# Performance work log

Measured on AMD Instinct MI355X. Metric: run time of the kernel, lower is better.

Reference implementation:

```python
import jax, jax.numpy as jnp
import numpy as np

EPS = 1e-5

def _bn(y, gamma, beta):
    # BatchNorm1d in training mode over the flattened (B*N, C) batch dim.
    m = jnp.mean(y, axis=0)
    v = jnp.var(y, axis=0)  # biased variance, matches torch normalization
    return gamma * (y - m) * jax.lax.rsqrt(v + EPS) + beta

def _hardswish(x):
    return x * jnp.clip(x + 3.0, 0.0, 6.0) / 6.0

def setup_inputs() -> dict:
    key = jax.random.key(0)
    ks = jax.random.split(key, 8)
    B, N, C, H = 16, 784, 384, 8
    res = int(N ** 0.5)  # 28
    inner = 3 * C
    x = jax.random.normal(ks[0], (B, N, C), dtype=jnp.float32)
    Wqkv = jax.random.normal(ks[1], (inner, C), dtype=jnp.float32) * (C ** -0.5)
    g1 = jnp.ones((inner,), jnp.float32) + 0.1 * jax.random.normal(ks[2], (inner,))
    b1 = 0.1 * jax.random.normal(ks[3], (inner,))
    Wproj = jax.random.normal(ks[4], (C, C), dtype=jnp.float32) * (C ** -0.5)
    g2 = jnp.ones((C,), jnp.float32) + 0.1 * jax.random.normal(ks[5], (C,))
    b2 = 0.1 * jax.random.normal(ks[6], (C,))
    biases = 0.02 * jax.random.normal(ks[7], (H, res * res), dtype=jnp.float32)
    # idx[i,j] = |dx|*res + |dy| reproduces torch's encounter-order offset ids
    coords = np.stack(np.meshgrid(np.arange(res), np.arange(res), indexing='ij'), -1).reshape(N, 2)
    d = np.abs(coords[:, None, :] - coords[None, :, :])
    bias_idxs = jnp.asarray(d[..., 0] * res + d[..., 1], dtype=jnp.int32)  # [N,N]
    return {"x": x, "Wqkv": Wqkv, "g1": g1, "b1": b1, "Wproj": Wproj,
            "g2": g2, "b2": b2, "biases": biases, "bias_idxs": bias_idxs}

def reference(x, Wqkv, g1, b1, Wproj, g2, b2, biases, bias_idxs):
    B, N, C = x.shape
    H = biases.shape[0]
    hd = C // H
    scale = hd ** -0.5
    # qkv = LinearNorm(dim, 3*dim)
    y = _bn(x.reshape(B * N, C) @ Wqkv.T, g1, b1)              # [B*N, 3C]
    qkv = y.reshape(B, N, 3, H, hd).transpose(2, 0, 3, 1, 4)   # [3,B,H,N,hd]
    q, k, v = qkv[0], qkv[1], qkv[2]
    attn = jnp.einsum('bhnd,bhmd->bhnm', q, k) * scale         # [B,H,N,N]
    attn = attn + biases[:, bias_idxs][None]                   # gathered rel-pos bias
    attn = jax.nn.softmax(attn, axis=-1)
    o = jnp.einsum('bhnm,bhmd->bhnd', attn, v)                 # [B,H,N,hd]
    o = o.transpose(0, 2, 1, 3).reshape(B, N, C)
    # proj = Hardswish -> LinearNorm(dim, dim)
    o = _hardswish(o).reshape(B * N, C)
    o = _bn(o @ Wproj.T, g2, b2)
    return o.reshape(B, N, C)
```

## Files before the change

### kernel.cpp

```cpp
#include <hip/hip_runtime.h>

#define R_TOTAL 12544
#define NTOK    784
#define CDIM    384
#define INNER   1152
#define NHEAD   8
#define HDIM    48
#define BATCH   16
#define SCALE   0.14433756729740643f
#define INV28   0.035714287f

typedef unsigned short u16;
typedef unsigned int   u32;
typedef __attribute__((ext_vector_type(8))) short short8;
typedef __attribute__((ext_vector_type(4))) float floatx4;

union V8 { uint4 u; short8 s; u16 h[8]; };

#define OB_OFF     28901376ull
#define ST_OFF     38535168ull

__device__ __forceinline__ float b2f(u16 u) {
    union { float f; u32 i; } v; v.i = ((u32)u) << 16; return v.f;
}
__device__ __forceinline__ u16 f2b(float f) {
    union { float f; u32 i; } v; v.f = f;
    u32 r = v.i + 0x7FFFu + ((v.i >> 16) & 1u);
    return (u16)(r >> 16);
}
__device__ __forceinline__ u32 pk2(float lo, float hi) {
    return (u32)f2b(lo) | ((u32)f2b(hi) << 16);
}
__device__ __forceinline__ float hswish_f(float v) {
    return v * fminf(fmaxf(v + 3.f, 0.f), 6.f) * (1.f / 6.f);
}

__global__ __launch_bounds__(256) void zero_k(float* __restrict__ p, int n) {
    int i = blockIdx.x * 256 + threadIdx.x;
    if (i < n) p[i] = 0.f;
}

template<int ABF16, int HSW, int OBF16>
__global__ __launch_bounds__(256) void gemm_mfma_k(
    const void* __restrict__ Ap, const float* __restrict__ Bfp,
    void* __restrict__ Cp, float* __restrict__ sums, int M, int Nout, int K)
{
    __shared__ u16 As[128 * 40];
    __shared__ u16 Bs[128 * 40];
    const int t = threadIdx.x;
    const int lane = t & 63, wv = t >> 6;
    const int l15 = lane & 15, quad = lane >> 4;
    const int wm = (wv & 1) * 64, wn = (wv >> 1) * 64;
    const int m0 = blockIdx.y * 128, n0 = blockIdx.x * 128;
    const floatx4 zf = {0.f, 0.f, 0.f, 0.f};

    floatx4 acc[4][4];
    #pragma unroll
    for (int i = 0; i < 4; i++)
        #pragma unroll
        for (int j = 0; j < 4; j++) acc[i][j] = zf;

    for (int k0 = 0; k0 < K; k0 += 32) {
        __syncthreads();
        #pragma unroll
        for (int it = 0; it < 2; it++) {
            const int flat = t + it * 256;
            const int rr = flat >> 2, ss = (flat & 3) * 8;
            uint4 aw;
            if (ABF16) {
                uint4 u = *(const uint4*)((const u16*)Ap + (size_t)(m0 + rr) * K + k0 + ss);
                if (HSW) {
                    aw.x = pk2(hswish_f(b2f((u16)(u.x & 0xffff))), hswish_f(b2f((u16)(u.x >> 16))));
                    aw.y = pk2(hswish_f(b2f((u16)(u.y & 0xffff))), hswish_f(b2f((u16)(u.y >> 16))));
                    aw.z = pk2(hswish_f(b2f((u16)(u.z & 0xffff))), hswish_f(b2f((u16)(u.z >> 16))));
                    aw.w = pk2(hswish_f(b2f((u16)(u.w & 0xffff))), hswish_f(b2f((u16)(u.w >> 16))));
                } else {
                    aw = u;
                }
            } else {
                const float* p = (const float*)Ap + (size_t)(m0 + rr) * K + k0 + ss;
                float4 f0 = *(const float4*)p, f1 = *(const float4*)(p + 4);
                aw.x = pk2(f0.x, f0.y); aw.y = pk2(f0.z, f0.w);
                aw.z = pk2(f1.x, f1.y); aw.w = pk2(f1.z, f1.w);
            }
            *(uint4*)&As[rr * 40 + ss] = aw;
            const float* q = Bfp + (size_t)(n0 + rr) * K + k0 + ss;
            float4 g0 = *(const float4*)q, g1 = *(const float4*)(q + 4);
            uint4 bw;
            bw.x = pk2(g0.x, g0.y); bw.y = pk2(g0.z, g0.w);
            bw.z = pk2(g1.x, g1.y); bw.w = pk2(g1.z, g1.w);
            *(uint4*)&Bs[rr * 40 + ss] = bw;
        }
        __syncthreads();
        short8 af[4], bfr[4];
        #pragma unroll
        for (int mi = 0; mi < 4; mi++)
            af[mi] = *(const short8*)&As[(wm + mi * 16 + l15) * 40 + quad * 8];
        #pragma unroll
        for (int ni = 0; ni < 4; ni++)
            bfr[ni] = *(const short8*)&Bs[(wn + ni * 16 + l15) * 40 + quad * 8];
        #pragma unroll
        for (int mi = 0; mi < 4; mi++)
            #pragma unroll
            for (int ni = 0; ni < 4; ni++)
                acc[mi][ni] = __builtin_amdgcn_mfma_f32_16x16x32_bf16(af[mi], bfr[ni], acc[mi][ni], 0, 0, 0);
    }

    float cs[4] = {0.f, 0.f, 0.f, 0.f}, cq[4] = {0.f, 0.f, 0.f, 0.f};
    #pragma unroll
    for (int mi = 0; mi < 4; mi++) {
        const int mbase = m0 + wm + mi * 16 + quad * 4;
        #pragma unroll
        for (int ni = 0; ni < 4; ni++) {
            const int n = n0 + wn + ni * 16 + l15;
            #pragma unroll
            for (int reg = 0; reg < 4; reg++) {
                size_t off = (size_t)(mbase + reg) * Nout + n;
                float v = acc[mi][ni][reg];
                float vv;
                if (OBF16) {
                    u16 hv = f2b(v);
                    ((u16*)Cp)[off] = hv;
                    vv = b2f(hv);
                } else {
                    ((float*)Cp)[off] = v;
                    vv = v;
                }
                cs[ni] += vv;
                cq[ni] += vv * vv;
            }
        }
    }
    #pragma unroll
    for (int ni = 0; ni < 4; ni++) {
        float s = cs[ni], sq = cq[ni];
        s  += __shfl_xor(s, 16);  s  += __shfl_xor(s, 32);
        sq += __shfl_xor(sq, 16); sq += __shfl_xor(sq, 32);
        if (quad == 0) {
            int col = n0 + wn + ni * 16 + l15;
            atomicAdd(&sums[col], s);
            atomicAdd(&sums[Nout + col], sq);
        }
    }
}

__global__ __launch_bounds__(256) void finalize_bn_k(
    const float* __restrict__ sums, const float* __restrict__ g,
    const float* __restrict__ bvec, float* __restrict__ ab, int Ncols, float invM)
{
    int c = blockIdx.x * 256 + threadIdx.x;
    if (c >= Ncols) return;
    float mean = sums[c] * invM;
    float var  = sums[Ncols + c] * invM - mean * mean;
    float a    = g[c] * rsqrtf(var + 1e-5f);
    ab[c] = a;
    ab[Ncols + c] = bvec[c] - mean * a;
}

__global__ __launch_bounds__(256) void bn_apply_k(
    float* __restrict__ Z, const float* __restrict__ ab, int Ncols, int total4)
{
    for (int i4 = blockIdx.x * 256 + threadIdx.x; i4 < total4; i4 += gridDim.x * 256) {
        int col = (i4 * 4) % Ncols;
        float4 z  = *(float4*)(Z + (size_t)i4 * 4);
        float4 a4 = *(const float4*)(ab + col);
        float4 b4 = *(const float4*)(ab + Ncols + col);
        z.x = a4.x * z.x + b4.x; z.y = a4.y * z.y + b4.y;
        z.z = a4.z * z.z + b4.z; z.w = a4.w * z.w + b4.w;
        *(float4*)(Z + (size_t)i4 * 4) = z;
    }
}

__global__ __launch_bounds__(256) void bn_apply_bf16_k(
    u16* __restrict__ Z, const float* __restrict__ ab, int Ncols, int total8)
{
    int i8 = blockIdx.x * 256 + threadIdx.x;
    if (i8 >= total8) return;
    int col = (i8 * 8) % Ncols;
    uint4 u = *(uint4*)(Z + (size_t)i8 * 8);
    float4 A0 = *(const float4*)(ab + col),         A1 = *(const float4*)(ab + col + 4);
    float4 B0 = *(const float4*)(ab + Ncols + col), B1 = *(const float4*)(ab + Ncols + col + 4);
    uint4 o;
    o.x = pk2(fmaf(b2f((u16)(u.x & 0xffff)), A0.x, B0.x), fmaf(b2f((u16)(u.x >> 16)), A0.y, B0.y));
    o.y = pk2(fmaf(b2f((u16)(u.y & 0xffff)), A0.z, B0.z), fmaf(b2f((u16)(u.y >> 16)), A0.w, B0.w));
    o.z = pk2(fmaf(b2f((u16)(u.z & 0xffff)), A1.x, B1.x), fmaf(b2f((u16)(u.z >> 16)), A1.y, B1.y));
    o.w = pk2(fmaf(b2f((u16)(u.w & 0xffff)), A1.z, B1.z), fmaf(b2f((u16)(u.w >> 16)), A1.w, B1.w));
    *(uint4*)(Z + (size_t)i8 * 8) = o;
}

__device__ __forceinline__ uint4 transpose8x8_u16(uint4 v, int g) {
    u32 r0 = v.x, r1 = v.y, r2 = v.z, r3 = v.w;
    {
        u32 t0 = (u32)__shfl_xor((int)r2, 4);
        u32 t1 = (u32)__shfl_xor((int)r3, 4);
        u32 t2 = (u32)__shfl_xor((int)r0, 4);
        u32 t3 = (u32)__shfl_xor((int)r1, 4);
        bool gb2 = (g >> 2) & 1;
        r0 = gb2 ? t0 : r0;
        r1 = gb2 ? t1 : r1;
        r2 = gb2 ? r2 : t2;
        r3 = gb2 ? r3 : t3;
    }
    {
        u32 t0 = (u32)__shfl_xor((int)r1, 2);
        u32 t1 = (u32)__shfl_xor((int)r0, 2);
        u32 t2 = (u32)__shfl_xor((int)r3, 2);
        u32 t3 = (u32)__shfl_xor((int)r2, 2);
        bool gb1 = (g >> 1) & 1;
        r0 = gb1 ? t0 : r0;
        r1 = gb1 ? r1 : t1;
        r2 = gb1 ? t2 : r2;
        r3 = gb1 ? r3 : t3;
    }
    {
        u32 t0 = (u32)__shfl_xor((int)r0, 1);
        u32 t1 = (u32)__shfl_xor((int)r1, 1);
        u32 t2 = (u32)__shfl_xor((int)r2, 1);
        u32 t3 = (u32)__shfl_xor((int)r3, 1);
        if (g & 1) {
            r0 = (r0 & 0xFFFF0000u) | (t0 >> 16);
            r1 = (r1 & 0xFFFF0000u) | (t1 >> 16);
            r2 = (r2 & 0xFFFF0000u) | (t2 >> 16);
            r3 = (r3 & 0xFFFF0000u) | (t3 >> 16);
        } else {
            r0 = (r0 & 0x0000FFFFu) | (t0 << 16);
            r1 = (r1 & 0x0000FFFFu) | (t1 << 16);
            r2 = (r2 & 0x0000FFFFu) | (t2 << 16);
            r3 = (r3 & 0x0000FFFFu) | (t3 << 16);
        }
    }
    return make_uint4(r0, r1, r2, r3);
}

__global__ __launch_bounds__(256) void attn_mfma_k(
    const u16* __restrict__ Y,
    const float* __restrict__ biases,
    u16* __restrict__ O)
{
    __shared__ u16 vt[2][6 * 64 * 8];
    __shared__ u16 psm[4][2][2 * 64 * 8];
    __shared__ float hb[NTOK];

    const int t = threadIdx.x;
    const int lane = t & 63, wv = t >> 6;
    const int l15 = lane & 15, quad = lane >> 4;
    const int g8 = lane & 7, sg = lane >> 3;
    const int bh = blockIdx.x;
    const int b = bh >> 3, h = bh & 7;
    const int n0 = blockIdx.y * 128;
    const int bN = b * NTOK;
    const int colQ = h * HDIM, colK = CDIM + colQ, colV = 2 * CDIM + colQ;
    const floatx4 zf = {0.f, 0.f, 0.f, 0.f};

    if (t < 196) *(float4*)&hb[t << 2] = *(const float4*)(biases + (size_t)h * NTOK + (t << 2));

    int qv[2], qr[2], xi[2], yi[2];
    #pragma unroll
    for (int qh = 0; qh < 2; qh++) {
        qv[qh] = n0 + qh * 64 + wv * 16 + l15;
        qr[qh] = qv[qh] < NTOK ? qv[qh] : NTOK - 1;
        xi[qh] = (int)((float)qr[qh] * INV28);
        yi[qh] = qr[qh] - 28 * xi[qh];
    }

    short8 qf[2][2];
    #pragma unroll
    for (int qh = 0; qh < 2; qh++) {
        V8 a0, a1;
        a1.u = make_uint4(0u, 0u, 0u, 0u);
        const u16* src = Y + (size_t)(bN + qr[qh]) * INNER + colQ;
        a0.u = *(const uint4*)(src + quad * 8);
        if (quad < 2) a1.u = *(const uint4*)(src + 32 + quad * 8);
        qf[qh][0] = a0.s; qf[qh][1] = a1.s;
    }

    const bool ownB = (wv < 2);
    const int dsA = wv, dsB = 4 + wv;
    const int dA = dsA * 8 + g8, dB = dsB * 8 + g8;
    const int vaddrA = (((dA >> 4) * 2 + (sg >> 2)) * 64 + (sg & 3) * 16 + (dA & 15)) * 8;
    const int vaddrB = (((dB >> 4) * 2 + (sg >> 2)) * 64 + (sg & 3) * 16 + (dB & 15)) * 8;

    V8 pvA, pvB;
    {
        const u16* src = Y + (size_t)(bN + lane) * INNER + colV;
        pvA.u = *(const uint4*)(src + dsA * 8);
        if (ownB) pvB.u = *(const uint4*)(src + dsB * 8);
        *(uint4*)&vt[0][vaddrA] = transpose8x8_u16(pvA.u, g8);
        if (ownB) *(uint4*)&vt[0][vaddrB] = transpose8x8_u16(pvB.u, g8);
    }

    V8 kfr[4][2];
    #pragma unroll
    for (int sub = 0; sub < 4; sub++) {
        const u16* src = Y + (size_t)(bN + sub * 16 + l15) * INNER + colK;
        kfr[sub][0].u = *(const uint4*)(src + quad * 8);
        kfr[sub][1].u = *(const uint4*)(src + 32 + quad * 8);
    }

    float lsum[2] = {0.f, 0.f};
    floatx4 oacc[2][3];
    #pragma unroll
    for (int qh = 0; qh < 2; qh++)
        #pragma unroll
        for (int i = 0; i < 3; i++) oacc[qh][i] = zf;

    const int psbase = ((quad >> 1) * 16 + l15) * 8 + (quad & 1) * 4;

    for (int mt = 0; mt < 13; mt++) {
        const int m0k = mt * 64;
        __syncthreads();

        V8 kn[4][2];
        const bool more = (mt + 1 < 13);
        if (more) {
            const int mn = m0k + 64;
            #pragma unroll
            for (int sub = 0; sub < 4; sub++) {
                int key = mn + sub * 16 + l15;
                int kr  = key < NTOK ? key : NTOK - 1;
                const u16* src = Y + (size_t)(bN + kr) * INNER + colK;
                kn[sub][0].u = *(const uint4*)(src + quad * 8);
                kn[sub][1].u = *(const uint4*)(src + 32 + quad * 8);
            }
            int kv = mn + lane; kv = kv < NTOK ? kv : NTOK - 1;
            const u16* src = Y + (size_t)(bN + kv) * INNER + colV;
            pvA.u = *(const uint4*)(src + dsA * 8);
            if (ownB) pvB.u = *(const uint4*)(src + dsB * 8);
        }

        #pragma unroll
        for (int qh = 0; qh < 2; qh++) {
            floatx4 sf[4];
            #pragma unroll
            for (int sub = 0; sub < 4; sub++) {
                floatx4 c = zf;
                c = __builtin_amdgcn_mfma_f32_16x16x32_bf16(kfr[sub][0].s, qf[qh][0], c, 0, 0, 0);
                c = __builtin_amdgcn_mfma_f32_16x16x32_bf16(kfr[sub][1].s, qf[qh][1], c, 0, 0, 0);
                sf[sub] = c;
            }
            #pragma unroll
            for (int sub = 0; sub < 4; sub++) {
                int kb = m0k + sub * 16 + quad * 4;
                float pr[4];
                #pragma unroll
                for (int reg = 0; reg < 4; reg++) {
                    int key = kb + reg;
                    int xk = (int)((float)key * INV28);
                    int yk = key - 28 * xk;
                    int dx = xi[qh] - xk; dx = dx < 0 ? -dx : dx;
                    int dy = yi[qh] - yk; dy = dy < 0 ? -dy : dy;
                    float p = 0.f;
                    if (key < NTOK)
                        p = __expf(fmaf(sf[sub][reg], SCALE, hb[dx * 28 + dy]));
                    pr[reg] = p;
                    lsum[qh] += p;
                }
                int addr = psbase + (sub >> 1) * 512 + (sub & 1) * 256;
                *(uint2*)&psm[wv][qh][addr] = make_uint2(pk2(pr[0], pr[1]), pk2(pr[2], pr[3]));
            }
        }

        if (more) {
            u16* vtb = vt[(mt + 1) & 1];
            *(uint4*)&vtb[vaddrA] = transpose8x8_u16(pvA.u, g8);
            if (ownB) *(uint4*)&vtb[vaddrB] = transpose8x8_u16(pvB.u, g8);
        }

        const u16* vtb = vt[mt & 1];
        #pragma unroll
        for (int kc = 0; kc < 2; kc++) {
            short8 pb0 = *(const short8*)&psm[wv][0][(kc * 64 + lane) * 8];
            short8 pb1 = *(const short8*)&psm[wv][1][(kc * 64 + lane) * 8];
            #pragma unroll
            for (int ns = 0; ns < 3; ns++) {
                short8 va = *(const short8*)&vtb[((ns * 2 + kc) * 64 + lane) * 8];
                oacc[0][ns] = __builtin_amdgcn_mfma_f32_16x16x32_bf16(va, pb0, oacc[0][ns], 0, 0, 0);
                oacc[1][ns] = __builtin_amdgcn_mfma_f32_16x16x32_bf16(va, pb1, oacc[1][ns], 0, 0, 0);
            }
        }

        if (more) {
            #pragma unroll
            for (int sub = 0; sub < 4; sub++) {
                kfr[sub][0] = kn[sub][0];
                kfr[sub][1] = kn[sub][1];
            }
        }
    }

    #pragma unroll
    for (int qh = 0; qh < 2; qh++) {
        float ls = lsum[qh];
        ls += __shfl_xor(ls, 16);
        ls += __shfl_xor(ls, 32);
        if (qv[qh] < NTOK) {
            float rl = 1.f / ls;
            u16* dst = O + (size_t)(bN + qv[qh]) * CDIM + colQ;
            #pragma unroll
            for (int ns = 0; ns < 3; ns++)
                #pragma unroll
                for (int reg = 0; reg < 4; reg++)
                    dst[ns * 16 + quad * 4 + reg] = f2b(hswish_f(oacc[qh][ns][reg] * rl));
        }
    }
}

extern "C" void kernel_launch(void* const* d_in, const int* in_sizes, int n_in,
                              void* d_out, int out_size, void* d_ws, size_t ws_size,
                              hipStream_t stream)
{
    const float* x     = (const float*)d_in[0];
    const float* Wqkv  = (const float*)d_in[1];
    const float* g1    = (const float*)d_in[2];
    const float* b1    = (const float*)d_in[3];
    const float* Wproj = (const float*)d_in[4];
    const float* g2    = (const float*)d_in[5];
    const float* b2    = (const float*)d_in[6];
    const float* bias  = (const float*)d_in[7];
    float* out = (float*)d_out;
    char*  wsb = (char*)d_ws;

    u16*   Yb  = (u16*)wsb;
    u16*   Ob  = (u16*)(wsb + OB_OFF);
    float* S1  = (float*)(wsb + ST_OFF);
    float* AB1 = S1 + 2304;
    float* S2  = AB1 + 2304;
    float* AB2 = S2 + 768;

    zero_k<<<24, 256, 0, stream>>>(S1, 6144);

    gemm_mfma_k<0, 0, 1><<<dim3(INNER / 128, R_TOTAL / 128), 256, 0, stream>>>(
        x, Wqkv, Yb, S1, R_TOTAL, INNER, CDIM);

    finalize_bn_k<<<(INNER + 255) / 256, 256, 0, stream>>>(S1, g1, b1, AB1, INNER, 1.f / R_TOTAL);
    bn_apply_bf16_k<<<(R_TOTAL * INNER / 8 + 255) / 256, 256, 0, stream>>>(
        Yb, AB1, INNER, R_TOTAL * INNER / 8);

    attn_mfma_k<<<dim3(NHEAD * BATCH, 7), 256, 0, stream>>>(Yb, bias, Ob);

    gemm_mfma_k<1, 0, 0><<<dim3(CDIM / 128, R_TOTAL / 128), 256, 0, stream>>>(
        Ob, Wproj, out, S2, R_TOTAL, CDIM, CDIM);

    finalize_bn_k<<<(CDIM + 255) / 256, 256, 0, stream>>>(S2, g2, b2, AB2, CDIM, 1.f / R_TOTAL);
    bn_apply_k<<<1024, 256, 0, stream>>>(out, AB2, CDIM, (R_TOTAL * CDIM) / 4);
}
```

Baseline: 259.5 us.

## Fold softmax scale and log2e into K BN; use raw v_exp and index table

Folds the attention scale times log2(e) into the batch-norm affine coefficients of the K columns, and multiplies the bias table by log2(e), so the softmax can call the hardware base-2 exp directly. Replaces the per-element integer divide-by-28 coordinate math with loads from the provided bias index table, moves the key-range mask to the last tile only, and packs bf16 pairs with a single perm instruction. This cuts ALU work in the softmax inner loop. In exchange it adds global int4 index loads per tile and applies the scale before bf16 rounding of K, which slightly changes numerics.

```diff
diff --git a/kernel.cpp b/kernel.cpp
--- a/kernel.cpp
+++ b/kernel.cpp
@@ -8,7 +8,8 @@
 #define HDIM    48
 #define BATCH   16
 #define SCALE   0.14433756729740643f
-#define INV28   0.035714287f
+#define LOG2E   1.4426950408889634f
+#define SCLOG2E 0.20823509f
 
 typedef unsigned short u16;
 typedef unsigned int   u32;
@@ -29,7 +30,10 @@
     return (u16)(r >> 16);
 }
 __device__ __forceinline__ u32 pk2(float lo, float hi) {
-    return (u32)f2b(lo) | ((u32)f2b(hi) << 16);
+    union { float f; u32 i; } a, b; a.f = lo; b.f = hi;
+    u32 ra = a.i + 0x7FFFu + ((a.i >> 16) & 1u);
+    u32 rb = b.i + 0x7FFFu + ((b.i >> 16) & 1u);
+    return __builtin_amdgcn_perm(rb, ra, 0x07060302u);
 }
 __device__ __forceinline__ float hswish_f(float v) {
     return v * fminf(fmaxf(v + 3.f, 0.f), 6.f) * (1.f / 6.f);
@@ -146,15 +150,17 @@
 
 __global__ __launch_bounds__(256) void finalize_bn_k(
     const float* __restrict__ sums, const float* __restrict__ g,
-    const float* __restrict__ bvec, float* __restrict__ ab, int Ncols, float invM)
+    const float* __restrict__ bvec, float* __restrict__ ab, int Ncols, float invM,
+    int sc0, int sc1, float sfac)
 {
     int c = blockIdx.x * 256 + threadIdx.x;
     if (c >= Ncols) return;
     float mean = sums[c] * invM;
     float var  = sums[Ncols + c] * invM - mean * mean;
     float a    = g[c] * rsqrtf(var + 1e-5f);
-    ab[c] = a;
-    ab[Ncols + c] = bvec[c] - mean * a;
+    float f    = (c >= sc0 && c < sc1) ? sfac : 1.f;
+    ab[c] = a * f;
+    ab[Ncols + c] = (bvec[c] - mean * a) * f;
 }
 
 __global__ __launch_bounds__(256) void bn_apply_k(
@@ -234,7 +240,7 @@
 
 __global__ __launch_bounds__(256) void attn_mfma_k(
     const u16* __restrict__ Y,
-    const float* __restrict__ biases,
+    const float* __restrict__ biases, const int* __restrict__ idxs,
     u16* __restrict__ O)
 {
     __shared__ u16 vt[2][6 * 64 * 8];
@@ -252,16 +258,19 @@
     const int colQ = h * HDIM, colK = CDIM + colQ, colV = 2 * CDIM + colQ;
     const floatx4 zf = {0.f, 0.f, 0.f, 0.f};
 
-    if (t < 196) *(float4*)&hb[t << 2] = *(const float4*)(biases + (size_t)h * NTOK + (t << 2));
-
-    int qv[2], qr[2], xi[2], yi[2];
+    if (t < 196) {
+        float4 v = *(const float4*)(biases + (size_t)h * NTOK + (t << 2));
+        v.x *= LOG2E; v.y *= LOG2E; v.z *= LOG2E; v.w *= LOG2E;
+        *(float4*)&hb[t << 2] = v;
+    }
+
+    int qv[2], qr[2];
     #pragma unroll
     for (int qh = 0; qh < 2; qh++) {
         qv[qh] = n0 + qh * 64 + wv * 16 + l15;
         qr[qh] = qv[qh] < NTOK ? qv[qh] : NTOK - 1;
-        xi[qh] = (int)((float)qr[qh] * INV28);
-        yi[qh] = qr[qh] - 28 * xi[qh];
-    }
+    }
+    const int* idxrow[2] = { idxs + (size_t)qr[0] * NTOK, idxs + (size_t)qr[1] * NTOK };
 
     short8 qf[2][2];
     #pragma unroll
@@ -308,7 +317,18 @@
 
     for (int mt = 0; mt < 13; mt++) {
         const int m0k = mt * 64;
+        const bool tail = (m0k == 768);
         __syncthreads();
+
+        int4 ivc[2][4];
+        #pragma unroll
+        for (int qh = 0; qh < 2; qh++)
+            #pragma unroll
+            for (int sub = 0; sub < 4; sub++) {
+                int kb = m0k + sub * 16 + quad * 4;
+                kb = kb < NTOK - 4 ? kb : NTOK - 4;
+                ivc[qh][sub] = *(const int4*)(idxrow[qh] + kb);
+            }
 
         V8 kn[4][2];
         const bool more = (mt + 1 < 13);
@@ -340,21 +360,23 @@
             }
             #pragma unroll
             for (int sub = 0; sub < 4; sub++) {
-                int kb = m0k + sub * 16 + quad * 4;
+                const int4 iv = ivc[qh][sub];
+                float a0 = sf[sub][0] + hb[iv.x];
+                float a1 = sf[sub][1] + hb[iv.y];
+                float a2 = sf[sub][2] + hb[iv.z];
+                float a3 = sf[sub][3] + hb[iv.w];
                 float pr[4];
-                #pragma unroll
-                for (int reg = 0; reg < 4; reg++) {
-                    int key = kb + reg;
-                    int xk = (int)((float)key * INV28);
-                    int yk = key - 28 * xk;
-                    int dx = xi[qh] - xk; dx = dx < 0 ? -dx : dx;
-                    int dy = yi[qh] - yk; dy = dy < 0 ? -dy : dy;
-                    float p = 0.f;
-                    if (key < NTOK)
-                        p = __expf(fmaf(sf[sub][reg], SCALE, hb[dx * 28 + dy]));
-                    pr[reg] = p;
-                    lsum[qh] += p;
+                asm("v_exp_f32 %0, %1" : "=v"(pr[0]) : "v"(a0));
+                asm("v_exp_f32 %0, %1" : "=v"(pr[1]) : "v"(a1));
+                asm("v_exp_f32 %0, %1" : "=v"(pr[2]) : "v"(a2));
+                asm("v_exp_f32 %0, %1" : "=v"(pr[3]) : "v"(a3));
+                if (tail) {
+                    const int kb0 = m0k + sub * 16 + quad * 4;
+                    #pragma unroll
+                    for (int reg = 0; reg < 4; reg++)
+                        if (kb0 + reg >= NTOK) pr[reg] = 0.f;
                 }
+                lsum[qh] += (pr[0] + pr[1]) + (pr[2] + pr[3]);
                 int addr = psbase + (sub >> 1) * 512 + (sub & 1) * 256;
                 *(uint2*)&psm[wv][qh][addr] = make_uint2(pk2(pr[0], pr[1]), pk2(pr[2], pr[3]));
             }
@@ -417,6 +439,7 @@
     const float* g2    = (const float*)d_in[5];
     const float* b2    = (const float*)d_in[6];
     const float* bias  = (const float*)d_in[7];
+    const int*   idxs  = (const int*)d_in[8];
     float* out = (float*)d_out;
     char*  wsb = (char*)d_ws;
 
@@ -432,15 +455,17 @@
     gemm_mfma_k<0, 0, 1><<<dim3(INNER / 128, R_TOTAL / 128), 256, 0, stream>>>(
         x, Wqkv, Yb, S1, R_TOTAL, INNER, CDIM);
 
-    finalize_bn_k<<<(INNER + 255) / 256, 256, 0, stream>>>(S1, g1, b1, AB1, INNER, 1.f / R_TOTAL);
+    finalize_bn_k<<<(INNER + 255) / 256, 256, 0, stream>>>(
+        S1, g1, b1, AB1, INNER, 1.f / R_TOTAL, CDIM, 2 * CDIM, SCLOG2E);
     bn_apply_bf16_k<<<(R_TOTAL * INNER / 8 + 255) / 256, 256, 0, stream>>>(
         Yb, AB1, INNER, R_TOTAL * INNER / 8);
 
-    attn_mfma_k<<<dim3(NHEAD * BATCH, 7), 256, 0, stream>>>(Yb, bias, Ob);
+    attn_mfma_k<<<dim3(NHEAD * BATCH, 7), 256, 0, stream>>>(Yb, bias, idxs, Ob);
 
     gemm_mfma_k<1, 0, 0><<<dim3(CDIM / 128, R_TOTAL / 128), 256, 0, stream>>>(
         Ob, Wproj, out, S2, R_TOTAL, CDIM, CDIM);
 
-    finalize_bn_k<<<(CDIM + 255) / 256, 256, 0, stream>>>(S2, g2, b2, AB2, CDIM, 1.f / R_TOTAL);
+    finalize_bn_k<<<(CDIM + 255) / 256, 256, 0, stream>>>(
+        S2, g2, b2, AB2, CDIM, 1.f / R_TOTAL, 0, 0, 1.f);
     bn_apply_k<<<1024, 256, 0, stream>>>(out, AB2, CDIM, (R_TOTAL * CDIM) / 4);
 }
```

New measurement: 251.3 us. -3.2%, faster.
